# Optimization experiments

Measured on AMD Instinct MI355X. Metric: run time of the kernel, lower is better.

Reference implementation:

```python
import jax, jax.numpy as jnp
import numpy as np

H = 1024   # d_model
N = 64     # state size (N//2 complex modes)
L_VAL = 4096
DT_MIN, DT_MAX = 1e-3, 0.1


def setup_inputs() -> dict:
    key = jax.random.key(0)
    k1, k2 = jax.random.split(key, 2)
    log_dt = (jax.random.uniform(k1, (H,), dtype=jnp.float32)
              * (np.float32(np.log(DT_MAX)) - np.float32(np.log(DT_MIN)))
              + np.float32(np.log(DT_MIN)))
    C_real = jax.random.normal(k2, (H, N // 2, 2), dtype=jnp.float32)
    # parameterization='exp': log_A_real = log(0.5)
    log_A_real = jnp.full((H, N // 2), np.float32(np.log(0.5)), dtype=jnp.float32)
    A_imag = np.float32(np.pi) * jnp.broadcast_to(
        jnp.arange(N // 2, dtype=jnp.float32), (H, N // 2))
    return {"C_real": C_real, "log_dt": log_dt, "log_A_real": log_A_real,
            "A_imag": A_imag, "L": L_VAL}


def reference(C_real, log_dt, log_A_real, A_imag, L):
    dt = jnp.exp(log_dt)                              # (H,)
    C = C_real[..., 0] + 1j * C_real[..., 1]          # (H, N/2) complex
    A = -jnp.exp(log_A_real) + 1j * A_imag            # (H, N/2) complex ('exp' param)
    dtA = A * dt[:, None]                             # (H, N/2)
    # C <- C * (exp(dtA) - 1) / A
    Ct = C * (jnp.exp(dtA) - 1.0) / A                 # (H, N/2)
    # Vandermonde: exp(dtA[:, :, None] * arange(L)) -> (H, N/2, L)
    V = jnp.exp(dtA[:, :, None] * jnp.arange(L, dtype=jnp.float32))
    K = 2.0 * jnp.einsum('hn,hnl->hl', Ct, V).real    # (H, L) real
    return K
```

## Files before the change

kernel.cpp:

```cpp
#include <hip/hip_runtime.h>
#include <math.h>

#define NMODES 32
#define INV2PI 0.15915494309189535f

typedef short bf16x8 __attribute__((ext_vector_type(8)));
typedef float f32x4  __attribute__((ext_vector_type(4)));

__device__ inline void sincos_rev(float rev, float& s, float& c) {
    float f = rev - floorf(rev);
    s = __builtin_amdgcn_sinf(f);
    c = __builtin_amdgcn_cosf(f);
}

__device__ inline void split_bf(float x, short& hi, short& lo) {
    const unsigned u = __float_as_uint(x);
    const float xf = __uint_as_float(u & 0xFFFF0000u);
    hi = (short)(u >> 16);
    const float r = x - xf;
    lo = (short)(__float_as_uint(r) >> 16);
}

__global__ __launch_bounds__(64) void ssm_mfma_kernel(
    const float* __restrict__ C_real,
    const float* __restrict__ log_dt,
    const float* __restrict__ log_A_real,
    const float* __restrict__ A_imag,
    float* __restrict__ K,
    int L)
{
    const int h    = blockIdx.x;
    const int lane = threadIdx.x;
    const int r    = lane & 15;
    const int g    = lane >> 4;

    const float dt = __expf(log_dt[h]);

    bf16x8 Bh0[4], Bl0[4], Bh1[4], Bl1[4];
    float dAr_[8], rhi_[8], rlo_[8], Ctr_[8], Cti_[8];

#pragma unroll
    for (int j = 0; j < 8; ++j) {
        const int m   = g * 8 + j;
        const int idx = h * NMODES + m;
        const float Ar = -__expf(log_A_real[idx]);
        const float Ai = A_imag[idx];
        const float dAr = dt * Ar;
        const float dAi_rev = dt * Ai * INV2PI;

        const float rhi = __uint_as_float(__float_as_uint(dAi_rev) & 0xFFFFF000u);
        const float rlo = dAi_rev - rhi;

        float sn, cs;
        sincos_rev(dAi_rev, sn, cs);
        const float er   = __expf(dAr);
        const float em1r = er * cs - 1.0f;
        const float em1i = er * sn;
        const float inv  = 1.0f / (Ar * Ar + Ai * Ai);
        const float fr   = (em1r * Ar + em1i * Ai) * inv;
        const float fi   = (em1i * Ar - em1r * Ai) * inv;
        const float Cr   = C_real[idx * 2 + 0];
        const float Ci   = C_real[idx * 2 + 1];
        const float Ctr  = Cr * fr - Ci * fi;
        const float Cti  = Cr * fi + Ci * fr;

        dAr_[j] = dAr; rhi_[j] = rhi; rlo_[j] = rlo; Ctr_[j] = Ctr; Cti_[j] = Cti;

#pragma unroll
        for (int b = 0; b < 4; ++b) {
            const float d  = (float)(r + 16 * b);
            const float pm = __expf(dAr * d);
            const float p  = rhi * d;
            const float f  = (p - floorf(p)) + rlo * d;
            float qs, qc;
            sincos_rev(f, qs, qc);
            const float qr = pm * qc;
            const float qi = pm * qs;
            short hh, ll;
            split_bf(qr, hh, ll); Bh0[b][j] = hh; Bl0[b][j] = ll;
            split_bf(qi, hh, ll); Bh1[b][j] = hh; Bl1[b][j] = ll;
        }
    }

    float* __restrict__ Kh = K + (size_t)h * L;

#pragma unroll
    for (int a = 0; a < 4; ++a) {
        bf16x8 Ah0, Al0, Ah1, Al1;
#pragma unroll
        for (int j = 0; j < 8; ++j) {
            const float t  = (float)(64 * (r + 16 * a));
            const float pm = __expf(dAr_[j] * t);
            const float p  = rhi_[j] * t;
            const float f  = (p - floorf(p)) + rlo_[j] * t;
            float zs, zc;
            sincos_rev(f, zs, zc);
            const float gr  = (Ctr_[j] * zc - Cti_[j] * zs) * pm;
            const float gni = -(Ctr_[j] * zs + Cti_[j] * zc) * pm;
            short hh, ll;
            split_bf(gr, hh, ll);  Ah0[j] = hh; Al0[j] = ll;
            split_bf(gni, hh, ll); Ah1[j] = hh; Al1[j] = ll;
        }

#pragma unroll
        for (int b = 0; b < 4; ++b) {
            f32x4 acc = {0.f, 0.f, 0.f, 0.f};
            acc = __builtin_amdgcn_mfma_f32_16x16x32_bf16(Ah0, Bh0[b], acc, 0, 0, 0);
            acc = __builtin_amdgcn_mfma_f32_16x16x32_bf16(Ah1, Bh1[b], acc, 0, 0, 0);
            acc = __builtin_amdgcn_mfma_f32_16x16x32_bf16(Ah0, Bl0[b], acc, 0, 0, 0);
            acc = __builtin_amdgcn_mfma_f32_16x16x32_bf16(Ah1, Bl1[b], acc, 0, 0, 0);
            acc = __builtin_amdgcn_mfma_f32_16x16x32_bf16(Al0, Bh0[b], acc, 0, 0, 0);
            acc = __builtin_amdgcn_mfma_f32_16x16x32_bf16(Al1, Bh1[b], acc, 0, 0, 0);
#pragma unroll
            for (int reg = 0; reg < 4; ++reg) {
                Kh[64 * (16 * a + 4 * g + reg) + 16 * b + r] = 2.0f * acc[reg];
            }
        }
    }
}

extern "C" void kernel_launch(void* const* d_in, const int* in_sizes, int n_in,
                              void* d_out, int out_size, void* d_ws, size_t ws_size,
                              hipStream_t stream) {
    const float* C_real     = (const float*)d_in[0];
    const float* log_dt     = (const float*)d_in[1];
    const float* log_A_real = (const float*)d_in[2];
    const float* A_imag     = (const float*)d_in[3];
    float* K = (float*)d_out;

    const int H = in_sizes[1];
    const int L = out_size / H;

    ssm_mfma_kernel<<<H, 64, 0, stream>>>(
        C_real, log_dt, log_A_real, A_imag, K, L);
}
```

Measured before the change: 12.81 us.

## Split per-head work across four wavefronts sharing B fragments via LDS

Each block now runs four wavefronts instead of one. Each wave computes one quarter of the B Vandermonde fragments and one A fragment row. The B fragments are exchanged through shared memory so every wave can run its own row of MFMA tiles. This spreads the transcendental-heavy setup across more waves to raise parallelism and latency hiding, at the cost of LDS traffic, a block barrier, and the per-mode coefficient setup being repeated in every wave.

Result: slower. 14.16 us (+10.6%).

```diff
diff --git a/kernel.cpp b/kernel.cpp
--- a/kernel.cpp
+++ b/kernel.cpp
@@ -21,7 +21,7 @@
     lo = (short)(__float_as_uint(r) >> 16);
 }
 
-__global__ __launch_bounds__(64) void ssm_mfma_kernel(
+__global__ __launch_bounds__(256, 4) void ssm_mfma_kernel(
     const float* __restrict__ C_real,
     const float* __restrict__ log_dt,
     const float* __restrict__ log_A_real,
@@ -29,14 +29,17 @@
     float* __restrict__ K,
     int L)
 {
+    __shared__ bf16x8 ldsB[16][64];
+
     const int h    = blockIdx.x;
-    const int lane = threadIdx.x;
+    const int tid  = threadIdx.x;
+    const int w    = tid >> 6;
+    const int lane = tid & 63;
     const int r    = lane & 15;
     const int g    = lane >> 4;
 
     const float dt = __expf(log_dt[h]);
 
-    bf16x8 Bh0[4], Bl0[4], Bh1[4], Bl1[4];
     float dAr_[8], rhi_[8], rlo_[8], Ctr_[8], Cti_[8];
 
 #pragma unroll
@@ -61,35 +64,36 @@
         const float fi   = (em1i * Ar - em1r * Ai) * inv;
         const float Cr   = C_real[idx * 2 + 0];
         const float Ci   = C_real[idx * 2 + 1];
-        const float Ctr  = Cr * fr - Ci * fi;
-        const float Cti  = Cr * fi + Ci * fr;
+        Ctr_[j] = Cr * fr - Ci * fi;
+        Cti_[j] = Cr * fi + Ci * fr;
+        dAr_[j] = dAr; rhi_[j] = rhi; rlo_[j] = rlo;
+    }
 
-        dAr_[j] = dAr; rhi_[j] = rhi; rlo_[j] = rlo; Ctr_[j] = Ctr; Cti_[j] = Cti;
-
+    {
+        bf16x8 bh0, bl0, bh1, bl1;
+        const float d = (float)(r + 16 * w);
 #pragma unroll
-        for (int b = 0; b < 4; ++b) {
-            const float d  = (float)(r + 16 * b);
-            const float pm = __expf(dAr * d);
-            const float p  = rhi * d;
-            const float f  = (p - floorf(p)) + rlo * d;
+        for (int j = 0; j < 8; ++j) {
+            const float pm = __expf(dAr_[j] * d);
+            const float p  = rhi_[j] * d;
+            const float f  = (p - floorf(p)) + rlo_[j] * d;
             float qs, qc;
             sincos_rev(f, qs, qc);
-            const float qr = pm * qc;
-            const float qi = pm * qs;
             short hh, ll;
-            split_bf(qr, hh, ll); Bh0[b][j] = hh; Bl0[b][j] = ll;
-            split_bf(qi, hh, ll); Bh1[b][j] = hh; Bl1[b][j] = ll;
+            split_bf(pm * qc, hh, ll); bh0[j] = hh; bl0[j] = ll;
+            split_bf(pm * qs, hh, ll); bh1[j] = hh; bl1[j] = ll;
         }
+        ldsB[w * 4 + 0][lane] = bh0;
+        ldsB[w * 4 + 1][lane] = bl0;
+        ldsB[w * 4 + 2][lane] = bh1;
+        ldsB[w * 4 + 3][lane] = bl1;
     }
 
-    float* __restrict__ Kh = K + (size_t)h * L;
-
-#pragma unroll
-    for (int a = 0; a < 4; ++a) {
-        bf16x8 Ah0, Al0, Ah1, Al1;
+    bf16x8 Ah0, Al0, Ah1, Al1;
+    {
+        const float t = (float)(64 * (r + 16 * w));
 #pragma unroll
         for (int j = 0; j < 8; ++j) {
-            const float t  = (float)(64 * (r + 16 * a));
             const float pm = __expf(dAr_[j] * t);
             const float p  = rhi_[j] * t;
             const float f  = (p - floorf(p)) + rlo_[j] * t;
@@ -101,20 +105,28 @@
             split_bf(gr, hh, ll);  Ah0[j] = hh; Al0[j] = ll;
             split_bf(gni, hh, ll); Ah1[j] = hh; Al1[j] = ll;
         }
+    }
+
+    __syncthreads();
+
+    float* __restrict__ Kh = K + (size_t)h * L;
 
 #pragma unroll
-        for (int b = 0; b < 4; ++b) {
-            f32x4 acc = {0.f, 0.f, 0.f, 0.f};
-            acc = __builtin_amdgcn_mfma_f32_16x16x32_bf16(Ah0, Bh0[b], acc, 0, 0, 0);
-            acc = __builtin_amdgcn_mfma_f32_16x16x32_bf16(Ah1, Bh1[b], acc, 0, 0, 0);
-            acc = __builtin_amdgcn_mfma_f32_16x16x32_bf16(Ah0, Bl0[b], acc, 0, 0, 0);
-            acc = __builtin_amdgcn_mfma_f32_16x16x32_bf16(Ah1, Bl1[b], acc, 0, 0, 0);
-            acc = __builtin_amdgcn_mfma_f32_16x16x32_bf16(Al0, Bh0[b], acc, 0, 0, 0);
-            acc = __builtin_amdgcn_mfma_f32_16x16x32_bf16(Al1, Bh1[b], acc, 0, 0, 0);
+    for (int b = 0; b < 4; ++b) {
+        const bf16x8 Bh0 = ldsB[b * 4 + 0][lane];
+        const bf16x8 Bl0 = ldsB[b * 4 + 1][lane];
+        const bf16x8 Bh1 = ldsB[b * 4 + 2][lane];
+        const bf16x8 Bl1 = ldsB[b * 4 + 3][lane];
+        f32x4 acc = {0.f, 0.f, 0.f, 0.f};
+        acc = __builtin_amdgcn_mfma_f32_16x16x32_bf16(Ah0, Bh0, acc, 0, 0, 0);
+        acc = __builtin_amdgcn_mfma_f32_16x16x32_bf16(Ah1, Bh1, acc, 0, 0, 0);
+        acc = __builtin_amdgcn_mfma_f32_16x16x32_bf16(Ah0, Bl0, acc, 0, 0, 0);
+        acc = __builtin_amdgcn_mfma_f32_16x16x32_bf16(Ah1, Bl1, acc, 0, 0, 0);
+        acc = __builtin_amdgcn_mfma_f32_16x16x32_bf16(Al0, Bh0, acc, 0, 0, 0);
+        acc = __builtin_amdgcn_mfma_f32_16x16x32_bf16(Al1, Bh1, acc, 0, 0, 0);
 #pragma unroll
-            for (int reg = 0; reg < 4; ++reg) {
-                Kh[64 * (16 * a + 4 * g + reg) + 16 * b + r] = 2.0f * acc[reg];
-            }
+        for (int reg = 0; reg < 4; ++reg) {
+            Kh[64 * (16 * w + 4 * g + reg) + 16 * b + r] = 2.0f * acc[reg];
         }
     }
 }
@@ -131,6 +143,6 @@
     const int H = in_sizes[1];
     const int L = out_size / H;
 
-    ssm_mfma_kernel<<<H, 64, 0, stream>>>(
+    ssm_mfma_kernel<<<H, 256, 0, stream>>>(
         C_real, log_dt, log_A_real, A_imag, K, L);
 }
```

## Split each head across four blocks and swap MFMA operands for float4 stores

Applied to the files above, without the earlier changes.

The grid grows from H to 4H blocks, and each block computes one quarter of a head's L range (one 'a' tile), so more waves are resident to hide the transcendental work. MFMA operand order is swapped so each lane's accumulator holds four consecutive output elements, which allows a single float4 store in place of four strided scalar stores. Each block now recomputes the per-mode setup and the Q (fine Vandermonde) fragments, duplicating that work four times per head. Launch bounds request four blocks per CU.

After: 17.31 us. +35.1%, slower.

```diff
diff --git a/kernel.cpp b/kernel.cpp
--- a/kernel.cpp
+++ b/kernel.cpp
@@ -21,7 +21,7 @@
     lo = (short)(__float_as_uint(r) >> 16);
 }
 
-__global__ __launch_bounds__(64) void ssm_mfma_kernel(
+__global__ __launch_bounds__(64, 4) void ssm_mfma_kernel(
     const float* __restrict__ C_real,
     const float* __restrict__ log_dt,
     const float* __restrict__ log_A_real,
@@ -29,15 +29,18 @@
     float* __restrict__ K,
     int L)
 {
-    const int h    = blockIdx.x;
+    const int bid  = blockIdx.x;
+    const int h    = bid >> 2;
+    const int a    = bid & 3;
     const int lane = threadIdx.x;
     const int r    = lane & 15;
     const int g    = lane >> 4;
 
     const float dt = __expf(log_dt[h]);
+    const float t  = (float)(64 * (r + 16 * a));
 
-    bf16x8 Bh0[4], Bl0[4], Bh1[4], Bl1[4];
-    float dAr_[8], rhi_[8], rlo_[8], Ctr_[8], Cti_[8];
+    float dAr_[8], rhi_[8], rlo_[8];
+    bf16x8 Ah0, Al0, Ah1, Al1;
 
 #pragma unroll
     for (int j = 0; j < 8; ++j) {
@@ -64,58 +67,52 @@
         const float Ctr  = Cr * fr - Ci * fi;
         const float Cti  = Cr * fi + Ci * fr;
 
-        dAr_[j] = dAr; rhi_[j] = rhi; rlo_[j] = rlo; Ctr_[j] = Ctr; Cti_[j] = Cti;
+        const float pm = __expf(dAr * t);
+        const float p  = rhi * t;
+        const float f  = (p - floorf(p)) + rlo * t;
+        float zs, zc;
+        sincos_rev(f, zs, zc);
+        const float gr  = (Ctr * zc - Cti * zs) * pm;
+        const float gni = -(Ctr * zs + Cti * zc) * pm;
+        short hh, ll;
+        split_bf(gr, hh, ll);  Ah0[j] = hh; Al0[j] = ll;
+        split_bf(gni, hh, ll); Ah1[j] = hh; Al1[j] = ll;
 
+        dAr_[j] = dAr; rhi_[j] = rhi; rlo_[j] = rlo;
+    }
+
+    bf16x8 Qh0[4], Ql0[4], Qh1[4], Ql1[4];
 #pragma unroll
-        for (int b = 0; b < 4; ++b) {
-            const float d  = (float)(r + 16 * b);
-            const float pm = __expf(dAr * d);
-            const float p  = rhi * d;
-            const float f  = (p - floorf(p)) + rlo * d;
+    for (int b = 0; b < 4; ++b) {
+        const float d = (float)(r + 16 * b);
+#pragma unroll
+        for (int j = 0; j < 8; ++j) {
+            const float pm = __expf(dAr_[j] * d);
+            const float p  = rhi_[j] * d;
+            const float f  = (p - floorf(p)) + rlo_[j] * d;
             float qs, qc;
             sincos_rev(f, qs, qc);
-            const float qr = pm * qc;
-            const float qi = pm * qs;
             short hh, ll;
-            split_bf(qr, hh, ll); Bh0[b][j] = hh; Bl0[b][j] = ll;
-            split_bf(qi, hh, ll); Bh1[b][j] = hh; Bl1[b][j] = ll;
+            split_bf(pm * qc, hh, ll); Qh0[b][j] = hh; Ql0[b][j] = ll;
+            split_bf(pm * qs, hh, ll); Qh1[b][j] = hh; Ql1[b][j] = ll;
         }
     }
 
-    float* __restrict__ Kh = K + (size_t)h * L;
+    float* __restrict__ base = K + (size_t)h * L + 64 * (16 * a + r) + 4 * g;
 
 #pragma unroll
-    for (int a = 0; a < 4; ++a) {
-        bf16x8 Ah0, Al0, Ah1, Al1;
-#pragma unroll
-        for (int j = 0; j < 8; ++j) {
-            const float t  = (float)(64 * (r + 16 * a));
-            const float pm = __expf(dAr_[j] * t);
-            const float p  = rhi_[j] * t;
-            const float f  = (p - floorf(p)) + rlo_[j] * t;
-            float zs, zc;
-            sincos_rev(f, zs, zc);
-            const float gr  = (Ctr_[j] * zc - Cti_[j] * zs) * pm;
-            const float gni = -(Ctr_[j] * zs + Cti_[j] * zc) * pm;
-            short hh, ll;
-            split_bf(gr, hh, ll);  Ah0[j] = hh; Al0[j] = ll;
-            split_bf(gni, hh, ll); Ah1[j] = hh; Al1[j] = ll;
-        }
-
-#pragma unroll
-        for (int b = 0; b < 4; ++b) {
-            f32x4 acc = {0.f, 0.f, 0.f, 0.f};
-            acc = __builtin_amdgcn_mfma_f32_16x16x32_bf16(Ah0, Bh0[b], acc, 0, 0, 0);
-            acc = __builtin_amdgcn_mfma_f32_16x16x32_bf16(Ah1, Bh1[b], acc, 0, 0, 0);
-            acc = __builtin_amdgcn_mfma_f32_16x16x32_bf16(Ah0, Bl0[b], acc, 0, 0, 0);
-            acc = __builtin_amdgcn_mfma_f32_16x16x32_bf16(Ah1, Bl1[b], acc, 0, 0, 0);
-            acc = __builtin_amdgcn_mfma_f32_16x16x32_bf16(Al0, Bh0[b], acc, 0, 0, 0);
-            acc = __builtin_amdgcn_mfma_f32_16x16x32_bf16(Al1, Bh1[b], acc, 0, 0, 0);
-#pragma unroll
-            for (int reg = 0; reg < 4; ++reg) {
-                Kh[64 * (16 * a + 4 * g + reg) + 16 * b + r] = 2.0f * acc[reg];
-            }
-        }
+    for (int b = 0; b < 4; ++b) {
+        f32x4 acc = {0.f, 0.f, 0.f, 0.f};
+        acc = __builtin_amdgcn_mfma_f32_16x16x32_bf16(Qh0[b], Ah0, acc, 0, 0, 0);
+        acc = __builtin_amdgcn_mfma_f32_16x16x32_bf16(Qh1[b], Ah1, acc, 0, 0, 0);
+        acc = __builtin_amdgcn_mfma_f32_16x16x32_bf16(Ql0[b], Ah0, acc, 0, 0, 0);
+        acc = __builtin_amdgcn_mfma_f32_16x16x32_bf16(Ql1[b], Ah1, acc, 0, 0, 0);
+        acc = __builtin_amdgcn_mfma_f32_16x16x32_bf16(Qh0[b], Al0, acc, 0, 0, 0);
+        acc = __builtin_amdgcn_mfma_f32_16x16x32_bf16(Qh1[b], Al1, acc, 0, 0, 0);
+        float4 o;
+        o.x = 2.0f * acc[0]; o.y = 2.0f * acc[1];
+        o.z = 2.0f * acc[2]; o.w = 2.0f * acc[3];
+        *(float4*)(base + 16 * b) = o;
     }
 }
 
@@ -131,6 +128,6 @@
     const int H = in_sizes[1];
     const int L = out_size / H;
 
-    ssm_mfma_kernel<<<H, 64, 0, stream>>>(
+    ssm_mfma_kernel<<<H * 4, 64, 0, stream>>>(
         C_real, log_dt, log_A_real, A_imag, K, L);
 }
```
